# Optimization experiments

Measured on AMD Instinct MI355X. Metric: run time of the kernel, lower is better.

## Reference

```python
import jax, jax.numpy as jnp
import numpy as np


def setup_inputs() -> dict:
    key = jax.random.key(0)
    k1, k2 = jax.random.split(key)
    predict = jax.random.normal(k1, (4, 8192, 3), dtype=jnp.float32)
    target = jax.random.normal(k2, (4, 8192, 3), dtype=jnp.float32)
    return {"predict": predict, "target": target}


def _chamfer(predict, target):
    xx = jnp.sum(predict * predict, axis=-1)  # [B, N]
    yy = jnp.sum(target * target, axis=-1)    # [B, M]
    xy = jnp.einsum("bnd,bmd->bnm", predict, target)  # [B, N, M]
    d = xx[:, :, None] + yy[:, None, :] - 2.0 * xy     # [B, N, M]
    x_near = jnp.min(d, axis=2)  # nearest target for each predict point, [B, N]
    y_near = jnp.min(d, axis=1)  # nearest predict for each target point, [B, M]
    return x_near.mean() + y_near.mean()


def reference(predict, target):
    return _chamfer(predict, target)
```

## Files before the change

### kernel.cpp

```cpp
#include <hip/hip_runtime.h>


#define NPTS   8192
#define NB     4
#define HALF   32768
#define NROWS  65536
#define NCHUNK 16
#define CW     512
#define P      8
#define RPB    2048
#define NRB    32

__global__ __launch_bounds__(256) void pack_kernel(
    const float* __restrict__ predict, const float* __restrict__ target,
    float4* __restrict__ packed)
{
    int r = blockIdx.x * 256 + threadIdx.x;
    const float* src = (r < HALF) ? (predict + (size_t)r * 3)
                                  : (target + (size_t)(r - HALF) * 3);
    float x = src[0], y = src[1], z = src[2];
    float nrm = fmaf(x, x, fmaf(y, y, z * z));
    packed[r] = make_float4(x, y, z, nrm);
}

__global__ __launch_bounds__(256) void minpart_kernel(
    const float4* __restrict__ packed, float* __restrict__ partial)
{
    __shared__ float4 sm[CW];
    const int rb   = blockIdx.x >> 4;
    const int cb   = blockIdx.x & (NCHUNK - 1);
    const int row0 = rb * RPB;
    const int sideA = (row0 < HALF) ? 1 : 0;
    const int local = sideA ? row0 : row0 - HALF;
    const int b = local >> 13;
    const int colBase = (sideA ? HALF : 0) + (b << 13) + cb * CW;

    for (int i = threadIdx.x; i < CW; i += 256)
        sm[i] = packed[colBase + i];
    __syncthreads();

    float px[P], py[P], pz[P], mn[P];
    #pragma unroll
    for (int j = 0; j < P; ++j) {
        float4 p = packed[row0 + threadIdx.x + j * 256];
        px[j] = p.x; py[j] = p.y; pz[j] = p.z;
        mn[j] = 3.4e38f;
    }

    #pragma unroll 4
    for (int i = 0; i < CW; ++i) {
        float4 t = sm[i];
        #pragma unroll
        for (int j = 0; j < P; ++j) {
            float dot = fmaf(px[j], t.x, fmaf(py[j], t.y, pz[j] * t.z));
            float s   = fmaf(-2.0f, dot, t.w);
            mn[j] = fminf(mn[j], s);
        }
    }

    #pragma unroll
    for (int j = 0; j < P; ++j)
        partial[(size_t)cb * NROWS + row0 + threadIdx.x + j * 256] = mn[j];
}

__global__ __launch_bounds__(256) void reduce_kernel(
    const float4* __restrict__ packed, const float* __restrict__ partial,
    float* __restrict__ blockSums)
{
    int r = blockIdx.x * 256 + threadIdx.x;
    float m = 3.4e38f;
    #pragma unroll
    for (int c = 0; c < NCHUNK; ++c)
        m = fminf(m, partial[(size_t)c * NROWS + r]);
    float val = m + packed[r].w;

    __shared__ float red[256];
    red[threadIdx.x] = val;
    __syncthreads();
    for (int s = 128; s > 0; s >>= 1) {
        if (threadIdx.x < s) red[threadIdx.x] += red[threadIdx.x + s];
        __syncthreads();
    }
    if (threadIdx.x == 0) blockSums[blockIdx.x] = red[0];
}

__global__ __launch_bounds__(256) void final_kernel(
    const float* __restrict__ blockSums, float* __restrict__ out)
{
    __shared__ float red[256];
    red[threadIdx.x] = blockSums[threadIdx.x];
    __syncthreads();
    for (int s = 128; s > 0; s >>= 1) {
        if (threadIdx.x < s) red[threadIdx.x] += red[threadIdx.x + s];
        __syncthreads();
    }
    if (threadIdx.x == 0) out[0] = red[0] * (1.0f / (float)HALF);
}

extern "C" void kernel_launch(void* const* d_in, const int* in_sizes, int n_in,
                              void* d_out, int out_size, void* d_ws, size_t ws_size,
                              hipStream_t stream)
{
    const float* predict = (const float*)d_in[0];
    const float* target  = (const float*)d_in[1];
    float* out = (float*)d_out;

    char* ws = (char*)d_ws;
    float4* packed   = (float4*)ws;
    float*  partial  = (float*)(ws + (size_t)NROWS * sizeof(float4));
    float*  blockSums = (float*)(ws + (size_t)NROWS * sizeof(float4)
                                    + (size_t)NROWS * NCHUNK * sizeof(float));

    pack_kernel   <<<NROWS / 256,  256, 0, stream>>>(predict, target, packed);
    minpart_kernel<<<NRB * NCHUNK, 256, 0, stream>>>(packed, partial);
    reduce_kernel <<<NROWS / 256,  256, 0, stream>>>(packed, partial, blockSums);
    final_kernel  <<<1,            256, 0, stream>>>(blockSums, out);
}
```

Baseline: 65.13 us.

## Fold -2 scale into query coords, use v_min3, and atomicMin row minima

The query coordinates are pre-scaled by -2 so each distance is three chained FMAs seeded with the target norm. The inner loop handles four targets per step and merges them with the v_min3_f32 instruction. The column split grows from 16 to 64 chunks, giving four times as many blocks for better occupancy. Per-chunk partial minima are replaced by atomicMin on order-preserving integer keys, which shrinks the partial buffer and the reduce pass at the cost of 64 atomics per row.

```diff
diff --git a/kernel.cpp b/kernel.cpp
--- a/kernel.cpp
+++ b/kernel.cpp
@@ -2,18 +2,32 @@
 
 
 #define NPTS   8192
-#define NB     4
 #define HALF   32768
 #define NROWS  65536
-#define NCHUNK 16
-#define CW     512
 #define P      8
 #define RPB    2048
 #define NRB    32
+#define NCH    64
+#define CW     (NPTS / NCH)
+
+__device__ __forceinline__ float min3f(float a, float b, float c) {
+    float d;
+    asm("v_min3_f32 %0, %1, %2, %3" : "=v"(d) : "v"(a), "v"(b), "v"(c));
+    return d;
+}
+
+__device__ __forceinline__ unsigned int fkey(float f) {
+    unsigned int b = __float_as_uint(f);
+    return (b & 0x80000000u) ? ~b : (b | 0x80000000u);
+}
+__device__ __forceinline__ float funkey(unsigned int k) {
+    unsigned int b = (k & 0x80000000u) ? (k ^ 0x80000000u) : ~k;
+    return __uint_as_float(b);
+}
 
 __global__ __launch_bounds__(256) void pack_kernel(
     const float* __restrict__ predict, const float* __restrict__ target,
-    float4* __restrict__ packed)
+    float4* __restrict__ packed, unsigned int* __restrict__ rowmin)
 {
     int r = blockIdx.x * 256 + threadIdx.x;
     const float* src = (r < HALF) ? (predict + (size_t)r * 3)
@@ -21,58 +35,61 @@
     float x = src[0], y = src[1], z = src[2];
     float nrm = fmaf(x, x, fmaf(y, y, z * z));
     packed[r] = make_float4(x, y, z, nrm);
+    rowmin[r] = 0xFFFFFFFFu;
 }
 
 __global__ __launch_bounds__(256) void minpart_kernel(
-    const float4* __restrict__ packed, float* __restrict__ partial)
+    const float4* __restrict__ packed, unsigned int* __restrict__ rowmin)
 {
     __shared__ float4 sm[CW];
-    const int rb   = blockIdx.x >> 4;
-    const int cb   = blockIdx.x & (NCHUNK - 1);
+    const int rb   = blockIdx.x / NCH;
+    const int cb   = blockIdx.x % NCH;
     const int row0 = rb * RPB;
-    const int sideA = (row0 < HALF) ? 1 : 0;
+    const bool sideA = (row0 < HALF);
     const int local = sideA ? row0 : row0 - HALF;
     const int b = local >> 13;
     const int colBase = (sideA ? HALF : 0) + (b << 13) + cb * CW;
 
-    for (int i = threadIdx.x; i < CW; i += 256)
-        sm[i] = packed[colBase + i];
+    if (threadIdx.x < CW)
+        sm[threadIdx.x] = packed[colBase + threadIdx.x];
     __syncthreads();
 
-    float px[P], py[P], pz[P], mn[P];
+    float qx[P], qy[P], qz[P], mn[P];
     #pragma unroll
     for (int j = 0; j < P; ++j) {
         float4 p = packed[row0 + threadIdx.x + j * 256];
-        px[j] = p.x; py[j] = p.y; pz[j] = p.z;
+        qx[j] = -2.0f * p.x; qy[j] = -2.0f * p.y; qz[j] = -2.0f * p.z;
         mn[j] = 3.4e38f;
     }
 
-    #pragma unroll 4
-    for (int i = 0; i < CW; ++i) {
-        float4 t = sm[i];
+    #pragma unroll 1
+    for (int i = 0; i < CW; i += 4) {
+        float4 t0 = sm[i + 0];
+        float4 t1 = sm[i + 1];
+        float4 t2 = sm[i + 2];
+        float4 t3 = sm[i + 3];
         #pragma unroll
         for (int j = 0; j < P; ++j) {
-            float dot = fmaf(px[j], t.x, fmaf(py[j], t.y, pz[j] * t.z));
-            float s   = fmaf(-2.0f, dot, t.w);
-            mn[j] = fminf(mn[j], s);
+            float s0 = fmaf(qx[j], t0.x, fmaf(qy[j], t0.y, fmaf(qz[j], t0.z, t0.w)));
+            float s1 = fmaf(qx[j], t1.x, fmaf(qy[j], t1.y, fmaf(qz[j], t1.z, t1.w)));
+            float s2 = fmaf(qx[j], t2.x, fmaf(qy[j], t2.y, fmaf(qz[j], t2.z, t2.w)));
+            float s3 = fmaf(qx[j], t3.x, fmaf(qy[j], t3.y, fmaf(qz[j], t3.z, t3.w)));
+            mn[j] = min3f(mn[j], s0, s1);
+            mn[j] = min3f(mn[j], s2, s3);
         }
     }
 
     #pragma unroll
     for (int j = 0; j < P; ++j)
-        partial[(size_t)cb * NROWS + row0 + threadIdx.x + j * 256] = mn[j];
+        atomicMin(&rowmin[row0 + threadIdx.x + j * 256], fkey(mn[j]));
 }
 
 __global__ __launch_bounds__(256) void reduce_kernel(
-    const float4* __restrict__ packed, const float* __restrict__ partial,
+    const float4* __restrict__ packed, const unsigned int* __restrict__ rowmin,
     float* __restrict__ blockSums)
 {
     int r = blockIdx.x * 256 + threadIdx.x;
-    float m = 3.4e38f;
-    #pragma unroll
-    for (int c = 0; c < NCHUNK; ++c)
-        m = fminf(m, partial[(size_t)c * NROWS + r]);
-    float val = m + packed[r].w;
+    float val = funkey(rowmin[r]) + packed[r].w;
 
     __shared__ float red[256];
     red[threadIdx.x] = val;
@@ -106,13 +123,13 @@
     float* out = (float*)d_out;
 
     char* ws = (char*)d_ws;
-    float4* packed   = (float4*)ws;
-    float*  partial  = (float*)(ws + (size_t)NROWS * sizeof(float4));
-    float*  blockSums = (float*)(ws + (size_t)NROWS * sizeof(float4)
-                                    + (size_t)NROWS * NCHUNK * sizeof(float));
+    float4*       packed    = (float4*)ws;
+    unsigned int* rowmin    = (unsigned int*)(ws + (size_t)NROWS * 16);
+    float*        blockSums = (float*)(ws + (size_t)NROWS * 16
+                                          + (size_t)NROWS * 4);
 
-    pack_kernel   <<<NROWS / 256,  256, 0, stream>>>(predict, target, packed);
-    minpart_kernel<<<NRB * NCHUNK, 256, 0, stream>>>(packed, partial);
-    reduce_kernel <<<NROWS / 256,  256, 0, stream>>>(packed, partial, blockSums);
-    final_kernel  <<<1,            256, 0, stream>>>(blockSums, out);
+    pack_kernel   <<<NROWS / 256, 256, 0, stream>>>(predict, target, packed, rowmin);
+    minpart_kernel<<<NRB * NCH,   256, 0, stream>>>(packed, rowmin);
+    reduce_kernel <<<NROWS / 256, 256, 0, stream>>>(packed, rowmin, blockSums);
+    final_kernel  <<<1,           256, 0, stream>>>(blockSums, out);
 }
```

Result: faster. 53.49 us (-17.9%).
